# Optimization experiments

Measured on AMD Instinct MI355X. Metric: run time of the kernel, lower is better.

## Reference

```python
import jax, jax.numpy as jnp
import numpy as np

# Block structure (mirrors init_kwargs)
K = 8            # number of blocks
BLK = 1024       # per-block in/out width
TOTAL = K * BLK  # total_dim = 8192
INPUT_IDX = [(i * BLK, (i + 1) * BLK) for i in range(K)]
OUTPUT_IDX = [(((i + 1) % K) * BLK, ((i + 1) % K + 1) * BLK) for i in range(K)]
BATCH = 4096


def setup_inputs() -> dict:
    key = jax.random.key(0)
    k1, k2, k3, k4 = jax.random.split(key, 4)
    x = jax.random.normal(k1, (BATCH, TOTAL), dtype=jnp.float32)
    v = jax.random.normal(k2, (BATCH, TOTAL), dtype=jnp.float32)
    # Per-block Linear params; nn.Linear default init ~ U(-1/sqrt(in), 1/sqrt(in))
    bound = 1.0 / np.sqrt(BLK)
    W = jax.random.uniform(k3, (K, BLK, BLK), dtype=jnp.float32, minval=-bound, maxval=bound)  # [K, out, in]
    b = jax.random.uniform(k4, (K, BLK), dtype=jnp.float32, minval=-bound, maxval=bound)
    return {"x": x, "v": v, "W": W, "b": b}


def reference(x, v, W, b):
    # hidden = act(v)
    hidden = jnp.tanh(v)
    # All input blocks are a uniform partition -> batch the K small GEMMs as one grouped contraction.
    h = hidden.reshape(BATCH, K, BLK)                      # [B, K, in]
    y = jnp.einsum("bki,koi->bko", h, W) + b               # [B, K, out]
    # Scatter-accumulate each block output into its padded position, plus residual x.
    result = x
    for i, (o0, o1) in enumerate(OUTPUT_IDX):
        result = result.at[:, o0:o1].add(y[:, i])
    return result
```

## Files before the change

kernel.cpp:

```cpp
#include <hip/hip_runtime.h>
#include <hip/hip_bf16.h>
#include <stdint.h>

#define BATCH 4096
#define KGRP  8
#define BLK   1024
#define TOTAL 8192

typedef __attribute__((ext_vector_type(8))) short short8;
typedef __attribute__((ext_vector_type(4))) float f32x4;

#define AS1 __attribute__((address_space(1)))
#define AS3 __attribute__((address_space(3)))


__device__ __forceinline__ unsigned short f2bf(float f) {
    union { float f; uint32_t u; } c; c.f = f;
    uint32_t u = c.u;
    u += 0x7fffu + ((u >> 16) & 1u);
    return (unsigned short)(u >> 16);
}

__device__ __forceinline__ float fast_tanh(float x) {
    float e = __expf(2.0f * x);
    return 1.0f - 2.0f / (e + 1.0f);
}


__global__ void k_prep(const float4* __restrict__ v, ushort4* __restrict__ H,
                       const float4* __restrict__ W, ushort4* __restrict__ Wb) {
    const int b = blockIdx.x;
    if (b < 2048) {
        const int n4 = BATCH * TOTAL / 4;
        for (int i = b * 256 + threadIdx.x; i < n4; i += 2048 * 256) {
            float4 f = v[i];
            ushort4 o;
            o.x = f2bf(fast_tanh(f.x)); o.y = f2bf(fast_tanh(f.y));
            o.z = f2bf(fast_tanh(f.z)); o.w = f2bf(fast_tanh(f.w));
            H[i] = o;
        }
    } else {
        const int n4 = KGRP * BLK * BLK / 4;
        for (int i = (b - 2048) * 256 + threadIdx.x; i < n4; i += 512 * 256) {
            float4 f = W[i];
            ushort4 o;
            o.x = f2bf(f.x); o.y = f2bf(f.y); o.z = f2bf(f.z); o.w = f2bf(f.w);
            Wb[i] = o;
        }
    }
}


__device__ __forceinline__ void gload16(const unsigned short* src, char* dst) {
    __builtin_amdgcn_global_load_lds((const AS1 uint32_t*)src, (AS3 uint32_t*)dst, 16, 0, 0);
}

template<int N> __device__ __forceinline__ void waitvm() {
    if constexpr (N == 0)      asm volatile("s_waitcnt vmcnt(0)" ::: "memory");
    else if constexpr (N == 1) asm volatile("s_waitcnt vmcnt(1)" ::: "memory");
    else if constexpr (N == 2) asm volatile("s_waitcnt vmcnt(2)" ::: "memory");
}

template<bool SA, bool SB, int W>
__device__ __forceinline__ void tile_body(int kt, char* ldsp,
                                          uint32_t aRowB, uint32_t bRowB, uint32_t kc,
                                          f32x4 (*acc)[4],
                                          const unsigned short* Asrc, const unsigned short* Bsrc,
                                          uint32_t sdst) {
    const uint32_t bufb = (uint32_t)(kt & 1) * 32768u;
    const uint32_t nbuf = bufb ^ 32768u;
    const char* Lb = ldsp + bufb;

    short8 bfr[4], am[2];

#pragma unroll
    for (int n = 0; n < 4; ++n)
        bfr[n] = *(const short8*)(Lb + bRowB + n * 1024 + kc);
#pragma unroll
    for (int i = 0; i < 2; ++i)
        am[i] = *(const short8*)(Lb + aRowB + i * 1024 + kc);
    if constexpr (SA) gload16(Asrc + (kt + 1) * 32, ldsp + nbuf + sdst);
#pragma unroll
    for (int i = 0; i < 2; ++i)
#pragma unroll
        for (int n = 0; n < 4; ++n)
            acc[i][n] = __builtin_amdgcn_mfma_f32_16x16x32_bf16(am[i], bfr[n], acc[i][n], 0, 0, 0);
    __builtin_amdgcn_s_barrier();
    __builtin_amdgcn_sched_barrier(0);

#pragma unroll
    for (int i = 0; i < 2; ++i)
        am[i] = *(const short8*)(Lb + aRowB + (2 + i) * 1024 + kc);
    if constexpr (SB) gload16(Bsrc + (kt + 2) * 32, ldsp + bufb + 16384u + sdst);
#pragma unroll
    for (int i = 0; i < 2; ++i)
#pragma unroll
        for (int n = 0; n < 4; ++n)
            acc[2 + i][n] = __builtin_amdgcn_mfma_f32_16x16x32_bf16(am[i], bfr[n], acc[2 + i][n], 0, 0, 0);
    if constexpr (W >= 0) {
        waitvm<W>();
        __builtin_amdgcn_s_barrier();
        __builtin_amdgcn_sched_barrier(0);
    }
}

__global__ __launch_bounds__(1024, 4)
void k_gemm(const unsigned short* __restrict__ H, const unsigned short* __restrict__ Wb,
            const float* __restrict__ x, const float* __restrict__ bias,
            float* __restrict__ out) {
    __shared__ __attribute__((aligned(1024))) char lds[135168];
    char* ldsp = lds;

    const int bid   = blockIdx.x;
    const int g     = bid & 7;
    const int slot  = bid >> 3;
    const int mtile = slot >> 2;
    const int ntile = slot & 3;

    const int tid  = threadIdx.x;
    const int lane = tid & 63;
    const int w    = tid >> 6;
    const int wr   = w >> 2;
    const int wc   = w & 3;

    const uint32_t kc    = ((uint32_t)((lane >> 4) ^ ((lane >> 1) & 3))) << 4;
    const uint32_t aRowB = (uint32_t)(wr * 64 + (lane & 15)) * 64u;
    const uint32_t bRowB = 16384u + (uint32_t)(wc * 64 + (lane & 15)) * 64u;

    const int sCol = ((lane & 3) ^ ((lane >> 3) & 3)) << 3;
    const unsigned short* Asrc = H + (size_t)(mtile * 256 + w * 16 + (lane >> 2)) * TOTAL
                                   + (size_t)g * BLK + sCol;
    const unsigned short* Bsrc = Wb + (size_t)g * BLK * BLK
                                    + (size_t)(ntile * 256 + w * 16 + (lane >> 2)) * BLK + sCol;
    const uint32_t sdst = (uint32_t)(w << 10);

    f32x4 acc[4][4];
#pragma unroll
    for (int m = 0; m < 4; ++m)
#pragma unroll
        for (int n = 0; n < 4; ++n) acc[m][n] = (f32x4){0.f, 0.f, 0.f, 0.f};

    gload16(Asrc + 0 * 32, ldsp + 0u + sdst);
    gload16(Bsrc + 0 * 32, ldsp + 16384u + sdst);
    gload16(Asrc + 1 * 32, ldsp + 32768u + sdst);
    gload16(Bsrc + 1 * 32, ldsp + 32768u + 16384u + sdst);
    waitvm<2>();
    __builtin_amdgcn_s_barrier();
    __builtin_amdgcn_sched_barrier(0);

    tile_body<false, true, 1>(0, ldsp, aRowB, bRowB, kc, acc, Asrc, Bsrc, sdst);
#pragma unroll 1
    for (int kt = 1; kt < 30; ++kt)
        tile_body<true, true, 1>(kt, ldsp, aRowB, bRowB, kc, acc, Asrc, Bsrc, sdst);
    tile_body<true, false, 0>(30, ldsp, aRowB, bRowB, kc, acc, Asrc, Bsrc, sdst);
    tile_body<false, false, -1>(31, ldsp, aRowB, bRowB, kc, acc, Asrc, Bsrc, sdst);

    const int gout = (g + 1) & 7;
    const int q    = lane >> 4;
    const int cl   = lane & 15;
    const int row0 = mtile * 256 + wr * 64;
    const int col0 = ntile * 256 + wc * 64;
    char* eb = ldsp + 65536u + (uint32_t)w * 4352u;
    const float4 bias4 = *(const float4*)&bias[g * BLK + col0 + cl * 4];

#pragma unroll
    for (int m = 0; m < 4; ++m) {
#pragma unroll
        for (int n = 0; n < 4; ++n)
#pragma unroll
            for (int j = 0; j < 4; ++j)
                *(float*)(eb + (q * 4 + j) * 272 + (n * 16 + cl) * 4) = acc[m][n][j];
        asm volatile("s_waitcnt lgkmcnt(0)" ::: "memory");
        __builtin_amdgcn_sched_barrier(0);
#pragma unroll
        for (int i = 0; i < 4; ++i) {
            f32x4 vv = *(const f32x4*)(eb + (q + 4 * i) * 272 + cl * 16);
            const int r = row0 + m * 16 + q + 4 * i;
            const size_t idx = (size_t)r * TOTAL + (size_t)gout * BLK + col0 + cl * 4;
            const float4 xv = *(const float4*)&x[idx];
            float4 o;
            o.x = xv.x + bias4.x + vv[0];
            o.y = xv.y + bias4.y + vv[1];
            o.z = xv.z + bias4.z + vv[2];
            o.w = xv.w + bias4.w + vv[3];
            *(float4*)&out[idx] = o;
        }
        asm volatile("s_waitcnt lgkmcnt(0)" ::: "memory");
        __builtin_amdgcn_sched_barrier(0);
    }
}


__global__ void k_naive(const float* __restrict__ x, const float* __restrict__ v,
                        const float* __restrict__ W, const float* __restrict__ b,
                        float* __restrict__ out) {
    __shared__ float hv[BLK];
    const int bid = blockIdx.x;
    const int quarter = bid & 3;
    const int g = (bid >> 2) & 7;
    const int row = bid >> 5;
    for (int i = threadIdx.x; i < BLK; i += 256)
        hv[i] = tanhf(v[(size_t)row * TOTAL + g * BLK + i]);
    __syncthreads();
    const int o = quarter * 256 + threadIdx.x;
    const float* wrow = W + ((size_t)g * BLK + o) * BLK;
    float s = 0.f;
    for (int i = 0; i < BLK; ++i) s += hv[i] * wrow[i];
    const size_t oi = (size_t)row * TOTAL + (size_t)((g + 1) & 7) * BLK + o;
    out[oi] = x[oi] + b[g * BLK + o] + s;
}


extern "C" void kernel_launch(void* const* d_in, const int* in_sizes, int n_in,
                              void* d_out, int out_size, void* d_ws, size_t ws_size,
                              hipStream_t stream) {
    const float* x = (const float*)d_in[0];
    const float* v = (const float*)d_in[1];
    const float* W = (const float*)d_in[2];
    const float* b = (const float*)d_in[3];
    float* out = (float*)d_out;

    const size_t needH = (size_t)BATCH * TOTAL * sizeof(unsigned short);
    const size_t needW = (size_t)KGRP * BLK * BLK * sizeof(unsigned short);

    if (ws_size >= needH + needW) {
        unsigned short* H  = (unsigned short*)d_ws;
        unsigned short* Wb = (unsigned short*)((char*)d_ws + needH);
        k_prep<<<2560, 256, 0, stream>>>((const float4*)v, (ushort4*)H,
                                         (const float4*)W, (ushort4*)Wb);
        k_gemm<<<512, 1024, 0, stream>>>(H, Wb, x, b, out);
    } else {
        k_naive<<<BATCH * KGRP * 4, 256, 0, stream>>>(x, v, W, b, out);
    }
}
```

Baseline: 158.8 us.

## Fuse tanh into GEMM A-load and overlap epilogue with next subtile

Removes the separate tanh/bf16 pass over v (and the bf16 H buffer in the workspace). The GEMM now loads fp32 v directly, applies tanh and the bf16 cast in registers, and writes the result into LDS. Each block now covers four 128-row subtiles with 512 threads. It ping-pongs two accumulator sets so the previous subtile's epilogue overlaps the current subtile's k-loop, and it prefetches the residual x into LDS asynchronously. This trades a full H write and read for per-tile tanh compute and heavier register use, with only 256 blocks on the GPU.

```diff
diff --git a/kernel.cpp b/kernel.cpp
--- a/kernel.cpp
+++ b/kernel.cpp
@@ -12,6 +12,9 @@
 
 #define AS1 __attribute__((address_space(1)))
 #define AS3 __attribute__((address_space(3)))
+
+#define LDS_XOFF   49152u
+#define LDS_EBOFF  114688u
 
 
 __device__ __forceinline__ unsigned short f2bf(float f) {
@@ -26,60 +29,76 @@
     return 1.0f - 2.0f / (e + 1.0f);
 }
 
-
-__global__ void k_prep(const float4* __restrict__ v, ushort4* __restrict__ H,
-                       const float4* __restrict__ W, ushort4* __restrict__ Wb) {
-    const int b = blockIdx.x;
-    if (b < 2048) {
-        const int n4 = BATCH * TOTAL / 4;
-        for (int i = b * 256 + threadIdx.x; i < n4; i += 2048 * 256) {
-            float4 f = v[i];
-            ushort4 o;
-            o.x = f2bf(fast_tanh(f.x)); o.y = f2bf(fast_tanh(f.y));
-            o.z = f2bf(fast_tanh(f.z)); o.w = f2bf(fast_tanh(f.w));
-            H[i] = o;
-        }
-    } else {
-        const int n4 = KGRP * BLK * BLK / 4;
-        for (int i = (b - 2048) * 256 + threadIdx.x; i < n4; i += 512 * 256) {
-            float4 f = W[i];
-            ushort4 o;
-            o.x = f2bf(f.x); o.y = f2bf(f.y); o.z = f2bf(f.z); o.w = f2bf(f.w);
-            Wb[i] = o;
-        }
-    }
-}
-
-
 __device__ __forceinline__ void gload16(const unsigned short* src, char* dst) {
     __builtin_amdgcn_global_load_lds((const AS1 uint32_t*)src, (AS3 uint32_t*)dst, 16, 0, 0);
 }
+__device__ __forceinline__ void gload4(const float* src, char* dst) {
+    __builtin_amdgcn_global_load_lds((const AS1 uint32_t*)src, (AS3 uint32_t*)dst, 4, 0, 0);
+}
 
 template<int N> __device__ __forceinline__ void waitvm() {
-    if constexpr (N == 0)      asm volatile("s_waitcnt vmcnt(0)" ::: "memory");
-    else if constexpr (N == 1) asm volatile("s_waitcnt vmcnt(1)" ::: "memory");
-    else if constexpr (N == 2) asm volatile("s_waitcnt vmcnt(2)" ::: "memory");
-}
-
-template<bool SA, bool SB, int W>
-__device__ __forceinline__ void tile_body(int kt, char* ldsp,
-                                          uint32_t aRowB, uint32_t bRowB, uint32_t kc,
-                                          f32x4 (*acc)[4],
-                                          const unsigned short* Asrc, const unsigned short* Bsrc,
-                                          uint32_t sdst) {
-    const uint32_t bufb = (uint32_t)(kt & 1) * 32768u;
-    const uint32_t nbuf = bufb ^ 32768u;
-    const char* Lb = ldsp + bufb;
-
+    if constexpr (N == 0)       asm volatile("s_waitcnt vmcnt(0)" ::: "memory");
+    else if constexpr (N == 2)  asm volatile("s_waitcnt vmcnt(2)" ::: "memory");
+    else if constexpr (N == 4)  asm volatile("s_waitcnt vmcnt(4)" ::: "memory");
+    else if constexpr (N == 6)  asm volatile("s_waitcnt vmcnt(6)" ::: "memory");
+    else if constexpr (N == 14) asm volatile("s_waitcnt vmcnt(14)" ::: "memory");
+}
+__device__ __forceinline__ void waitlgkm0() {
+    asm volatile("s_waitcnt lgkmcnt(0)" ::: "memory");
+}
+
+
+__global__ void k_wcast(const float4* __restrict__ W, ushort4* __restrict__ Wb) {
+    const int n4 = KGRP * BLK * BLK / 4;
+    for (int i = blockIdx.x * 256 + threadIdx.x; i < n4; i += 1024 * 256) {
+        float4 f = W[i];
+        ushort4 o;
+        o.x = f2bf(f.x); o.y = f2bf(f.y); o.z = f2bf(f.z); o.w = f2bf(f.w);
+        Wb[i] = o;
+    }
+}
+
+
+template<bool HASE, bool WRA, bool ISSV, bool ISSB, int W>
+__device__ __forceinline__ void body(int kt, char* ldsp,
+                                     const float* vsrcT, const unsigned short* BsrcT,
+                                     const float* xsrcP,
+                                     float4& va0, float4& va1,
+                                     uint32_t awOff, uint32_t aBase, uint32_t bBase,
+                                     uint32_t sdstB, int w, int lane,
+                                     f32x4 (*acc)[4]) {
+    const uint32_t cur = (uint32_t)(kt & 1) * 24576u;
+    const uint32_t oth = cur ^ 24576u;
+    const char* Lb = ldsp + cur;
+
+    if constexpr (WRA) {
+        short8 p;
+        p[0] = (short)f2bf(fast_tanh(va0.x)); p[1] = (short)f2bf(fast_tanh(va0.y));
+        p[2] = (short)f2bf(fast_tanh(va0.z)); p[3] = (short)f2bf(fast_tanh(va0.w));
+        p[4] = (short)f2bf(fast_tanh(va1.x)); p[5] = (short)f2bf(fast_tanh(va1.y));
+        p[6] = (short)f2bf(fast_tanh(va1.z)); p[7] = (short)f2bf(fast_tanh(va1.w));
+        *(short8*)(ldsp + oth + awOff) = p;
+    }
     short8 bfr[4], am[2];
-
 #pragma unroll
     for (int n = 0; n < 4; ++n)
-        bfr[n] = *(const short8*)(Lb + bRowB + n * 1024 + kc);
+        bfr[n] = *(const short8*)(Lb + bBase + n * 1024);
 #pragma unroll
     for (int i = 0; i < 2; ++i)
-        am[i] = *(const short8*)(Lb + aRowB + i * 1024 + kc);
-    if constexpr (SA) gload16(Asrc + (kt + 1) * 32, ldsp + nbuf + sdst);
+        am[i] = *(const short8*)(Lb + aBase + i * 2048);
+    if constexpr (HASE) {
+        const float* xs = xsrcP + (size_t)(kt >> 4) * 64 * TOTAL;
+#pragma unroll
+        for (int j = 0; j < 2; ++j) {
+            const int ci = (kt & 15) * 16 + w * 2 + j;
+            gload4(xs + (size_t)(ci >> 2) * TOTAL + (ci & 3) * 64 + lane,
+                   ldsp + LDS_XOFF + (uint32_t)ci * 256u);
+        }
+    }
+    if constexpr (ISSV) {
+        va0 = *(const float4*)(vsrcT + (size_t)(kt + 2) * 32);
+        va1 = *(const float4*)(vsrcT + (size_t)(kt + 2) * 32 + 4);
+    }
 #pragma unroll
     for (int i = 0; i < 2; ++i)
 #pragma unroll
@@ -90,32 +109,145 @@
 
 #pragma unroll
     for (int i = 0; i < 2; ++i)
-        am[i] = *(const short8*)(Lb + aRowB + (2 + i) * 1024 + kc);
-    if constexpr (SB) gload16(Bsrc + (kt + 2) * 32, ldsp + bufb + 16384u + sdst);
+        am[i] = *(const short8*)(Lb + aBase + (2 + i) * 2048);
+    if constexpr (ISSB) {
+        gload16(BsrcT + (size_t)(kt + 2) * 32, ldsp + cur + 8192u + sdstB);
+        gload16(BsrcT + (size_t)128 * BLK + (size_t)(kt + 2) * 32, ldsp + cur + 16384u + sdstB);
+    }
 #pragma unroll
     for (int i = 0; i < 2; ++i)
 #pragma unroll
         for (int n = 0; n < 4; ++n)
             acc[2 + i][n] = __builtin_amdgcn_mfma_f32_16x16x32_bf16(am[i], bfr[n], acc[2 + i][n], 0, 0, 0);
-    if constexpr (W >= 0) {
-        waitvm<W>();
+    waitlgkm0();
+    if constexpr (W >= 0) waitvm<W>();
+    __builtin_amdgcn_s_barrier();
+    __builtin_amdgcn_sched_barrier(0);
+}
+
+
+template<int H>
+__device__ __forceinline__ void flushhalf(f32x4 (*accP)[4], char* ldsp,
+                                          int w, int lane, int wr, int wc,
+                                          float4 bias4, float* out, size_t outRowBase) {
+    char* eb = ldsp + LDS_EBOFF + (uint32_t)w * 4352u;
+    const char* xl = ldsp + LDS_XOFF;
+    const int q = lane >> 4, cl = lane & 15;
+#pragma unroll
+    for (int mm = 0; mm < 2; ++mm) {
+        const int mabs = 2 * H + mm;
+#pragma unroll
+        for (int n = 0; n < 4; ++n)
+#pragma unroll
+            for (int j = 0; j < 4; ++j)
+                *(float*)(eb + (q * 4 + j) * 272 + (n * 16 + cl) * 4) = accP[mabs][n][j];
+        waitlgkm0();
+        __builtin_amdgcn_sched_barrier(0);
+#pragma unroll
+        for (int i = 0; i < 4; ++i) {
+            const int lr = mm * 32 + wr * 16 + q + 4 * i;
+            f32x4 vv = *(const f32x4*)(eb + (q + 4 * i) * 272 + cl * 16);
+            f32x4 xv = *(const f32x4*)(xl + lr * 1024 + wc * 256 + cl * 16);
+            const size_t idx = outRowBase + (size_t)lr * TOTAL + wc * 64 + cl * 4;
+            float4 o;
+            o.x = xv[0] + bias4.x + vv[0];
+            o.y = xv[1] + bias4.y + vv[1];
+            o.z = xv[2] + bias4.z + vv[2];
+            o.w = xv[3] + bias4.w + vv[3];
+            *(float4*)&out[idx] = o;
+        }
+        waitlgkm0();
+        __builtin_amdgcn_sched_barrier(0);
+    }
+}
+
+
+template<bool HASE>
+__device__ __forceinline__ void subtile(int mt, int mtP, char* ldsp,
+                                        const float* v, const unsigned short* Wb,
+                                        const float* x, float* out,
+                                        int g, int gout, int ntile,
+                                        int tid, int w, int lane, int wr, int wc,
+                                        uint32_t awOff, uint32_t aBase, uint32_t bBase,
+                                        uint32_t sdstB, const unsigned short* BsrcT,
+                                        float4 bias4,
+                                        f32x4 (*accC)[4], f32x4 (*accP)[4]) {
+#pragma unroll
+    for (int m = 0; m < 4; ++m)
+#pragma unroll
+        for (int n = 0; n < 4; ++n) accC[m][n] = (f32x4){0.f, 0.f, 0.f, 0.f};
+
+    const float* vsrcT = v + (size_t)(mt * 128 + (tid >> 2)) * TOTAL + (size_t)g * BLK + (tid & 3) * 8;
+    const float* xsrcP = x + (size_t)(mtP * 128) * TOTAL + (size_t)gout * BLK + ntile * 256;
+    const size_t outB0 = (size_t)(mtP * 128) * TOTAL + (size_t)gout * BLK + ntile * 256;
+    float4 va0, va1;
+
+    {
+        float4 t0a = *(const float4*)(vsrcT);
+        float4 t0b = *(const float4*)(vsrcT + 4);
+        va0 = *(const float4*)(vsrcT + 32);
+        va1 = *(const float4*)(vsrcT + 36);
+        gload16(BsrcT, ldsp + 8192u + sdstB);
+        gload16(BsrcT + (size_t)128 * BLK, ldsp + 16384u + sdstB);
+        gload16(BsrcT + 32, ldsp + 24576u + 8192u + sdstB);
+        gload16(BsrcT + (size_t)128 * BLK + 32, ldsp + 24576u + 16384u + sdstB);
+        short8 p;
+        p[0] = (short)f2bf(fast_tanh(t0a.x)); p[1] = (short)f2bf(fast_tanh(t0a.y));
+        p[2] = (short)f2bf(fast_tanh(t0a.z)); p[3] = (short)f2bf(fast_tanh(t0a.w));
+        p[4] = (short)f2bf(fast_tanh(t0b.x)); p[5] = (short)f2bf(fast_tanh(t0b.y));
+        p[6] = (short)f2bf(fast_tanh(t0b.z)); p[7] = (short)f2bf(fast_tanh(t0b.w));
+        *(short8*)(ldsp + awOff) = p;
+        waitlgkm0();
+        waitvm<0>();
         __builtin_amdgcn_s_barrier();
         __builtin_amdgcn_sched_barrier(0);
     }
-}
-
-__global__ __launch_bounds__(1024, 4)
-void k_gemm(const unsigned short* __restrict__ H, const unsigned short* __restrict__ Wb,
+
+#pragma unroll 1
+    for (int kt = 0; kt < 15; ++kt)
+        body<HASE, true, true, true, (HASE ? 6 : 4)>(kt, ldsp, vsrcT, BsrcT, xsrcP,
+            va0, va1, awOff, aBase, bBase, sdstB, w, lane, accC);
+    body<HASE, true, true, true, (HASE ? 2 : 4)>(15, ldsp, vsrcT, BsrcT, xsrcP,
+        va0, va1, awOff, aBase, bBase, sdstB, w, lane, accC);
+    if constexpr (HASE) {
+        flushhalf<0>(accP, ldsp, w, lane, wr, wc, bias4, out, outB0);
+        waitlgkm0();
+        __builtin_amdgcn_s_barrier();
+        __builtin_amdgcn_sched_barrier(0);
+    }
+    body<HASE, true, true, true, (HASE ? 14 : 4)>(16, ldsp, vsrcT, BsrcT, xsrcP,
+        va0, va1, awOff, aBase, bBase, sdstB, w, lane, accC);
+#pragma unroll 1
+    for (int kt = 17; kt < 30; ++kt)
+        body<HASE, true, true, true, (HASE ? 6 : 4)>(kt, ldsp, vsrcT, BsrcT, xsrcP,
+            va0, va1, awOff, aBase, bBase, sdstB, w, lane, accC);
+    body<HASE, true, false, false, (HASE ? 2 : 0)>(30, ldsp, vsrcT, BsrcT, xsrcP,
+        va0, va1, awOff, aBase, bBase, sdstB, w, lane, accC);
+    body<HASE, false, false, false, (HASE ? 0 : -1)>(31, ldsp, vsrcT, BsrcT, xsrcP,
+        va0, va1, awOff, aBase, bBase, sdstB, w, lane, accC);
+    if constexpr (HASE) {
+        flushhalf<1>(accP, ldsp, w, lane, wr, wc, bias4, out,
+                     outB0 + (size_t)64 * TOTAL);
+        waitlgkm0();
+        __builtin_amdgcn_s_barrier();
+        __builtin_amdgcn_sched_barrier(0);
+    }
+}
+
+
+__global__ __launch_bounds__(512, 2)
+void k_gemm(const float* __restrict__ v, const unsigned short* __restrict__ Wb,
             const float* __restrict__ x, const float* __restrict__ bias,
             float* __restrict__ out) {
-    __shared__ __attribute__((aligned(1024))) char lds[135168];
+    __shared__ __attribute__((aligned(1024))) char lds[149504];
     char* ldsp = lds;
 
     const int bid   = blockIdx.x;
     const int g     = bid & 7;
     const int slot  = bid >> 3;
-    const int mtile = slot >> 2;
     const int ntile = slot & 3;
+    const int mq    = slot >> 2;
+    const int gout  = (g + 1) & 7;
 
     const int tid  = threadIdx.x;
     const int lane = tid & 63;
@@ -124,69 +256,58 @@
     const int wc   = w & 3;
 
     const uint32_t kc    = ((uint32_t)((lane >> 4) ^ ((lane >> 1) & 3))) << 4;
-    const uint32_t aRowB = (uint32_t)(wr * 64 + (lane & 15)) * 64u;
-    const uint32_t bRowB = 16384u + (uint32_t)(wc * 64 + (lane & 15)) * 64u;
-
-    const int sCol = ((lane & 3) ^ ((lane >> 3) & 3)) << 3;
-    const unsigned short* Asrc = H + (size_t)(mtile * 256 + w * 16 + (lane >> 2)) * TOTAL
-                                   + (size_t)g * BLK + sCol;
-    const unsigned short* Bsrc = Wb + (size_t)g * BLK * BLK
-                                    + (size_t)(ntile * 256 + w * 16 + (lane >> 2)) * BLK + sCol;
-    const uint32_t sdst = (uint32_t)(w << 10);
-
-    f32x4 acc[4][4];
-#pragma unroll
-    for (int m = 0; m < 4; ++m)
-#pragma unroll
-        for (int n = 0; n < 4; ++n) acc[m][n] = (f32x4){0.f, 0.f, 0.f, 0.f};
-
-    gload16(Asrc + 0 * 32, ldsp + 0u + sdst);
-    gload16(Bsrc + 0 * 32, ldsp + 16384u + sdst);
-    gload16(Asrc + 1 * 32, ldsp + 32768u + sdst);
-    gload16(Bsrc + 1 * 32, ldsp + 32768u + 16384u + sdst);
-    waitvm<2>();
-    __builtin_amdgcn_s_barrier();
-    __builtin_amdgcn_sched_barrier(0);
-
-    tile_body<false, true, 1>(0, ldsp, aRowB, bRowB, kc, acc, Asrc, Bsrc, sdst);
-#pragma unroll 1
-    for (int kt = 1; kt < 30; ++kt)
-        tile_body<true, true, 1>(kt, ldsp, aRowB, bRowB, kc, acc, Asrc, Bsrc, sdst);
-    tile_body<true, false, 0>(30, ldsp, aRowB, bRowB, kc, acc, Asrc, Bsrc, sdst);
-    tile_body<false, false, -1>(31, ldsp, aRowB, bRowB, kc, acc, Asrc, Bsrc, sdst);
-
-    const int gout = (g + 1) & 7;
-    const int q    = lane >> 4;
-    const int cl   = lane & 15;
-    const int row0 = mtile * 256 + wr * 64;
-    const int col0 = ntile * 256 + wc * 64;
-    char* eb = ldsp + 65536u + (uint32_t)w * 4352u;
-    const float4 bias4 = *(const float4*)&bias[g * BLK + col0 + cl * 4];
-
-#pragma unroll
-    for (int m = 0; m < 4; ++m) {
-#pragma unroll
-        for (int n = 0; n < 4; ++n)
-#pragma unroll
-            for (int j = 0; j < 4; ++j)
-                *(float*)(eb + (q * 4 + j) * 272 + (n * 16 + cl) * 4) = acc[m][n][j];
-        asm volatile("s_waitcnt lgkmcnt(0)" ::: "memory");
-        __builtin_amdgcn_sched_barrier(0);
-#pragma unroll
-        for (int i = 0; i < 4; ++i) {
-            f32x4 vv = *(const f32x4*)(eb + (q + 4 * i) * 272 + cl * 16);
-            const int r = row0 + m * 16 + q + 4 * i;
-            const size_t idx = (size_t)r * TOTAL + (size_t)gout * BLK + col0 + cl * 4;
-            const float4 xv = *(const float4*)&x[idx];
-            float4 o;
-            o.x = xv.x + bias4.x + vv[0];
-            o.y = xv.y + bias4.y + vv[1];
-            o.z = xv.z + bias4.z + vv[2];
-            o.w = xv.w + bias4.w + vv[3];
-            *(float4*)&out[idx] = o;
+    const uint32_t aBase = (uint32_t)(wr * 16 + (lane & 15)) * 64u + kc;
+    const uint32_t bBase = 8192u + (uint32_t)(wc * 64 + (lane & 15)) * 64u + kc;
+    const uint32_t awOff = (uint32_t)((tid >> 2) * 64) +
+                           ((uint32_t)((tid & 3) ^ ((tid >> 3) & 3)) << 4);
+    const int sColB = ((lane & 3) ^ ((lane >> 3) & 3)) << 3;
+    const unsigned short* BsrcT = Wb + (size_t)g * BLK * BLK
+                                     + (size_t)(ntile * 256 + w * 16 + (lane >> 2)) * BLK + sColB;
+    const uint32_t sdstB = (uint32_t)(w << 10);
+
+    const float4 bias4 = *(const float4*)&bias[g * BLK + ntile * 256 + wc * 64 + (lane & 15) * 4];
+
+    f32x4 acc0[4][4], acc1[4][4];
+
+    subtile<false>(mq * 4 + 0, 0,          ldsp, v, Wb, x, out, g, gout, ntile,
+                   tid, w, lane, wr, wc, awOff, aBase, bBase, sdstB, BsrcT, bias4, acc0, acc1);
+    subtile<true >(mq * 4 + 1, mq * 4 + 0, ldsp, v, Wb, x, out, g, gout, ntile,
+                   tid, w, lane, wr, wc, awOff, aBase, bBase, sdstB, BsrcT, bias4, acc1, acc0);
+    subtile<true >(mq * 4 + 2, mq * 4 + 1, ldsp, v, Wb, x, out, g, gout, ntile,
+                   tid, w, lane, wr, wc, awOff, aBase, bBase, sdstB, BsrcT, bias4, acc0, acc1);
+    subtile<true >(mq * 4 + 3, mq * 4 + 2, ldsp, v, Wb, x, out, g, gout, ntile,
+                   tid, w, lane, wr, wc, awOff, aBase, bBase, sdstB, BsrcT, bias4, acc1, acc0);
+
+    {
+        const int mt3 = mq * 4 + 3;
+        char* eb = ldsp + LDS_EBOFF + (uint32_t)w * 4352u;
+        const int q = lane >> 4, cl = lane & 15;
+        const size_t base0 = (size_t)(mt3 * 128) * TOTAL + (size_t)gout * BLK + ntile * 256;
+#pragma unroll
+        for (int m = 0; m < 4; ++m) {
+#pragma unroll
+            for (int n = 0; n < 4; ++n)
+#pragma unroll
+                for (int j = 0; j < 4; ++j)
+                    *(float*)(eb + (q * 4 + j) * 272 + (n * 16 + cl) * 4) = acc1[m][n][j];
+            waitlgkm0();
+            __builtin_amdgcn_sched_barrier(0);
+#pragma unroll
+            for (int i = 0; i < 4; ++i) {
+                const int r = m * 32 + wr * 16 + q + 4 * i;
+                f32x4 vv = *(const f32x4*)(eb + (q + 4 * i) * 272 + cl * 16);
+                const size_t idx = base0 + (size_t)r * TOTAL + wc * 64 + cl * 4;
+                const float4 xv = *(const float4*)&x[idx];
+                float4 o;
+                o.x = xv.x + bias4.x + vv[0];
+                o.y = xv.y + bias4.y + vv[1];
+                o.z = xv.z + bias4.z + vv[2];
+                o.w = xv.w + bias4.w + vv[3];
+                *(float4*)&out[idx] = o;
+            }
+            waitlgkm0();
+            __builtin_amdgcn_sched_barrier(0);
         }
-        asm volatile("s_waitcnt lgkmcnt(0)" ::: "memory");
-        __builtin_amdgcn_sched_barrier(0);
     }
 }
 
@@ -220,15 +341,12 @@
     const float* b = (const float*)d_in[3];
     float* out = (float*)d_out;
 
-    const size_t needH = (size_t)BATCH * TOTAL * sizeof(unsigned short);
     const size_t needW = (size_t)KGRP * BLK * BLK * sizeof(unsigned short);
 
-    if (ws_size >= needH + needW) {
-        unsigned short* H  = (unsigned short*)d_ws;
-        unsigned short* Wb = (unsigned short*)((char*)d_ws + needH);
-        k_prep<<<2560, 256, 0, stream>>>((const float4*)v, (ushort4*)H,
-                                         (const float4*)W, (ushort4*)Wb);
-        k_gemm<<<512, 1024, 0, stream>>>(H, Wb, x, b, out);
+    if (ws_size >= needW) {
+        unsigned short* Wb = (unsigned short*)d_ws;
+        k_wcast<<<1024, 256, 0, stream>>>((const float4*)W, (ushort4*)Wb);
+        k_gemm<<<256, 512, 0, stream>>>(v, Wb, x, b, out);
     } else {
         k_naive<<<BATCH * KGRP * 4, 256, 0, stream>>>(x, v, W, b, out);
     }
```

Result: slower. 236.1 us (+48.7%).
